# Optimization experiments

Measured on AMD Instinct MI355X. Metric: run time of the kernel, lower is better.

The kernel has to match this reference:

```python
import jax, jax.numpy as jnp
import numpy as np

B, S, D, H, L, F = 1, 2048, 768, 12, 2, 3072
DH = D // H          # 64
W = 256              # one-sided sliding window (attention_window=512 total)
NC = S // W          # number of query chunks
VOCAB = 50265


def _ln(x, s, b, eps=1e-5):
    m = x.mean(-1, keepdims=True)
    v = ((x - m) ** 2).mean(-1, keepdims=True)
    return (x - m) / jnp.sqrt(v + eps) * s + b


def setup_inputs() -> dict:
    key = jax.random.key(0)
    ks = jax.random.split(key, 16)
    p = lambda k, sh: jax.random.normal(k, sh, jnp.float32) * 0.02
    return {
        "input_ids": jax.random.randint(ks[0], (B, S), 0, VOCAB),
        "attention_mask": jnp.ones((B, S), jnp.int32),
        "word_emb": p(ks[1], (VOCAB, D)),
        "pos_emb": p(ks[2], (S + 2, D)),          # roberta-style pos ids start at 2
        "type_emb": p(ks[3], (1, D)),
        "emb_ln_s": jnp.ones((D,), jnp.float32),
        "emb_ln_b": jnp.zeros((D,), jnp.float32),
        "Wqkv": p(ks[4], (L, 3, D, D)),
        "bqkv": jnp.zeros((L, 3, D), jnp.float32),
        "Wo": p(ks[5], (L, D, D)),
        "bo": jnp.zeros((L, D), jnp.float32),
        "ln1_s": jnp.ones((L, D), jnp.float32),
        "ln1_b": jnp.zeros((L, D), jnp.float32),
        "W1": p(ks[6], (L, D, F)),
        "b1": jnp.zeros((L, F), jnp.float32),
        "W2": p(ks[7], (L, F, D)),
        "b2": jnp.zeros((L, D), jnp.float32),
        "ln2_s": jnp.ones((L, D), jnp.float32),
        "ln2_b": jnp.zeros((L, D), jnp.float32),
        "pool_W": p(ks[8], (D, D)),
        "pool_b": jnp.zeros((D,), jnp.float32),
    }


def reference(input_ids, attention_mask, word_emb, pos_emb, type_emb,
              emb_ln_s, emb_ln_b, Wqkv, bqkv, Wo, bo, ln1_s, ln1_b,
              W1, b1, W2, b2, ln2_s, ln2_b, pool_W, pool_b):
    # ---- embeddings (roberta/longformer style) ----
    pos_ids = jnp.cumsum(attention_mask, axis=1) * attention_mask + 1  # padding_idx=1
    x = word_emb[input_ids] + pos_emb[pos_ids] + type_emb[0]
    x = _ln(x, emb_ln_s, emb_ln_b)

    # ---- banded-attention index/mask precompute (int constants) ----
    idx = jnp.arange(NC)[:, None] * W + jnp.arange(3 * W)[None, :]      # [NC, 3W] into padded seq
    rel = (jnp.arange(3 * W)[None, :] - W) - jnp.arange(W)[:, None]     # key_pos - query_pos
    band = (rel >= -W) & (rel <= W)                                      # [W, 3W]
    kmask = jnp.pad(attention_mask, ((0, 0), (W, W)))[:, idx].astype(bool)  # [B, NC, 3W]
    valid = band[None, None] & kmask[:, :, None, :]                      # [B, NC, W, 3W]

    inv_sqrt_dh = 1.0 / np.sqrt(DH)
    for l in range(L):
        qkv = jnp.einsum('bsd,tde->tbse', x, Wqkv[l]) + bqkv[l][:, None, None, :]
        q, k, v = [t.reshape(B, S, H, DH).transpose(0, 2, 1, 3) for t in qkv]  # [B,H,S,DH]
        qc = q.reshape(B, H, NC, W, DH)
        kp = jnp.pad(k, ((0, 0), (0, 0), (W, W), (0, 0)))
        vp = jnp.pad(v, ((0, 0), (0, 0), (W, W), (0, 0)))
        kc = kp[:, :, idx]                                               # [B,H,NC,3W,DH]
        vc = vp[:, :, idx]
        scores = jnp.einsum('bhcqd,bhckd->bhcqk', qc, kc) * inv_sqrt_dh  # [B,H,NC,W,3W]
        scores = jnp.where(valid[:, None], scores, -1e9)
        attn = jax.nn.softmax(scores, axis=-1)
        ctx = jnp.einsum('bhcqk,bhckd->bhcqd', attn, vc)
        ctx = ctx.reshape(B, H, S, DH).transpose(0, 2, 1, 3).reshape(B, S, D)
        x = _ln(x + ctx @ Wo[l] + bo[l], ln1_s[l], ln1_b[l])
        h = jax.nn.gelu(x @ W1[l] + b1[l], approximate=False)
        x = _ln(x + h @ W2[l] + b2[l], ln2_s[l], ln2_b[l])

    pooled = jnp.tanh(x[:, 0] @ pool_W + pool_b)
    return x, pooled
```

## Files before the change

### kernel.cpp

```cpp
#include <hip/hip_runtime.h>
#include <hip/hip_bf16.h>
#include <math.h>
#include <stddef.h>
#include <stdint.h>

typedef __hip_bfloat16 bf16;
typedef short bf16x8 __attribute__((ext_vector_type(8)));
typedef float f32x4 __attribute__((ext_vector_type(4)));

#define CS 2048
#define CD 768
#define CH 12
#define CDH 64
#define CF 3072
#define CW 256
#define CL 2
#define QKVN 2304
#define SDC ((size_t)CS * CD)

__device__ __forceinline__ void gload_lds16(const bf16* g, bf16* l) {
  __builtin_amdgcn_global_load_lds(
      (const __attribute__((address_space(1))) void*)g,
      (__attribute__((address_space(3))) void*)l, 16, 0, 0);
}

__device__ __forceinline__ unsigned short f2bu(float v) {
  bf16 b = __float2bfloat16(v);
  return *(unsigned short*)&b;
}

__device__ __forceinline__ float block_reduce_sum(float v, float* buf) {
  #pragma unroll
  for (int off = 32; off > 0; off >>= 1) v += __shfl_down(v, off, 64);
  int wid = threadIdx.x >> 6;
  __syncthreads();
  if ((threadIdx.x & 63) == 0) buf[wid] = v;
  __syncthreads();
  if (threadIdx.x == 0) buf[0] = buf[0] + buf[1] + buf[2] + buf[3];
  __syncthreads();
  return buf[0];
}

__global__ __launch_bounds__(256) void transpose_all(
    const float* __restrict__ Wqkv, const float* __restrict__ Wo,
    const float* __restrict__ W1, const float* __restrict__ W2,
    bf16* __restrict__ WqkvT, bf16* __restrict__ WoT,
    bf16* __restrict__ W1T, bf16* __restrict__ W2T) {
  __shared__ float tile[32][33];
  int b = blockIdx.x;
  const float* src; bf16* dst; int K, N, t;
  if (b < 3456) {
    int mat = b / 576; t = b % 576; K = 768; N = 768;
    src = Wqkv + (size_t)mat * 768 * 768; dst = WqkvT + (size_t)mat * 768 * 768;
  } else if (b < 4608) {
    b -= 3456; int mat = b / 576; t = b % 576; K = 768; N = 768;
    src = Wo + (size_t)mat * 768 * 768; dst = WoT + (size_t)mat * 768 * 768;
  } else if (b < 9216) {
    b -= 4608; int mat = b / 2304; t = b % 2304; K = 768; N = 3072;
    src = W1 + (size_t)mat * 768 * 3072; dst = W1T + (size_t)mat * 768 * 3072;
  } else {
    b -= 9216; int mat = b / 2304; t = b % 2304; K = 3072; N = 768;
    src = W2 + (size_t)mat * 3072 * 768; dst = W2T + (size_t)mat * 3072 * 768;
  }
  int nt = N / 32;
  int bn = (t % nt) * 32, bk = (t / nt) * 32;
  int tx = threadIdx.x & 31, ty = (threadIdx.x >> 5) & 7;
  #pragma unroll
  for (int i = 0; i < 32; i += 8)
    tile[ty + i][tx] = src[(size_t)(bk + ty + i) * N + bn + tx];
  __syncthreads();
  #pragma unroll
  for (int i = 0; i < 32; i += 8)
    dst[(size_t)(bn + ty + i) * K + bk + tx] = __float2bfloat16(tile[tx][ty + i]);
}

__global__ __launch_bounds__(256) void embed_ln_kernel(
    const int* __restrict__ ids, const int* __restrict__ mask,
    const float* __restrict__ wemb, const float* __restrict__ pemb,
    const float* __restrict__ temb, const float* __restrict__ gs,
    const float* __restrict__ gb, float* __restrict__ x, bf16* __restrict__ xb) {
  __shared__ float red[4];
  int srow = blockIdx.x;
  float ps = 0.f;
  for (int i = threadIdx.x; i <= srow; i += 256) ps += (float)mask[i];
  float tot = block_reduce_sum(ps, red);
  long long pid = (long long)((int)(tot + 0.5f) * mask[srow] + 1);
  long long id = ids[srow];
  float v[3];
  #pragma unroll
  for (int i = 0; i < 3; ++i) {
    int d = threadIdx.x + i * 256;
    v[i] = wemb[id * CD + d] + pemb[pid * CD + d] + temb[d];
  }
  float sum = v[0] + v[1] + v[2];
  sum = block_reduce_sum(sum, red);
  float mean = sum * (1.0f / CD);
  float sq = 0.f;
  #pragma unroll
  for (int i = 0; i < 3; ++i) { float c = v[i] - mean; sq += c * c; }
  sq = block_reduce_sum(sq, red);
  float rstd = rsqrtf(sq * (1.0f / CD) + 1e-5f);
  #pragma unroll
  for (int i = 0; i < 3; ++i) {
    int d = threadIdx.x + i * 256;
    float o = (v[i] - mean) * rstd * gs[d] + gb[d];
    x[(size_t)srow * CD + d] = o;
    xb[(size_t)srow * CD + d] = __float2bfloat16(o);
  }
}

template<int GELU, int OUTBF16, int SPLITS, int VTFUSE>
__global__ __launch_bounds__(256) void gemm_mfma(
    const bf16* __restrict__ A, const bf16* __restrict__ Bt,
    const float* __restrict__ bias, void* __restrict__ Cout,
    bf16* __restrict__ vTout, int M, int N, int Ktot) {
  __shared__ __align__(16) bf16 As[128 * 64];
  __shared__ __align__(16) bf16 Bs[128 * 64];
  const int tid = threadIdx.x;
  const int wave = tid >> 6, lane = tid & 63;
  const int m0 = blockIdx.y * 128, n0 = blockIdx.x * 128;
  const int wm = (wave & 1) * 64, wn = (wave >> 1) * 64;
  const int quad = lane >> 4, rsel = lane & 15;
  const int rx = rsel & 7;
  const int r_in = lane >> 3;
  const int chunk = lane & 7;
  const int gchunk = chunk ^ r_in;
  const int Klen = Ktot / SPLITS;
  const int koff = (SPLITS > 1) ? blockIdx.z * Klen : 0;

  f32x4 acc[4][4] = {};

  for (int k0 = 0; k0 < Klen; k0 += 64) {
    #pragma unroll
    for (int i = 0; i < 8; ++i) {
      int op = wave * 8 + i;
      if (op < 16) {
        int row = op * 8 + r_in;
        gload_lds16(A + (size_t)(m0 + row) * Ktot + koff + k0 + gchunk * 8, &As[op * 512]);
      } else {
        int row = (op - 16) * 8 + r_in;
        gload_lds16(Bt + (size_t)(n0 + row) * Ktot + koff + k0 + gchunk * 8, &Bs[(op - 16) * 512]);
      }
    }
    __syncthreads();
    #pragma unroll
    for (int kh = 0; kh < 2; ++kh) {
      bf16x8 af[4], bfr[4];
      int cq = ((kh << 2) | quad);
      #pragma unroll
      for (int i = 0; i < 4; ++i)
        af[i] = *(const bf16x8*)&As[(wm + i * 16 + rsel) * 64 + (cq ^ rx) * 8];
      #pragma unroll
      for (int j = 0; j < 4; ++j)
        bfr[j] = *(const bf16x8*)&Bs[(wn + j * 16 + rsel) * 64 + (cq ^ rx) * 8];
      #pragma unroll
      for (int i = 0; i < 4; ++i)
        #pragma unroll
        for (int j = 0; j < 4; ++j)
          acc[i][j] = __builtin_amdgcn_mfma_f32_16x16x32_bf16(af[i], bfr[j], acc[i][j], 0, 0, 0);
    }
    __syncthreads();
  }
  #pragma unroll
  for (int j = 0; j < 4; ++j) {
    int col = n0 + wn + j * 16 + rsel;
    float bv = (SPLITS == 1 || blockIdx.z == 0) ? bias[col] : 0.f;
    if (VTFUSE && col >= 1536) {
      #pragma unroll
      for (int i = 0; i < 4; ++i) {
        int rowb = m0 + wm + i * 16 + quad * 4;
        ushort4 pk;
        pk.x = f2bu(acc[i][j][0] + bv);
        pk.y = f2bu(acc[i][j][1] + bv);
        pk.z = f2bu(acc[i][j][2] + bv);
        pk.w = f2bu(acc[i][j][3] + bv);
        *(ushort4*)&vTout[(size_t)(col - 1536) * CS + rowb] = pk;
      }
    } else {
      #pragma unroll
      for (int i = 0; i < 4; ++i) {
        #pragma unroll
        for (int r = 0; r < 4; ++r) {
          int rowm = m0 + wm + i * 16 + quad * 4 + r;
          float v = acc[i][j][r] + bv;
          if (GELU) v = 0.5f * v * (1.0f + erff(v * 0.70710678118654752f));
          if (SPLITS > 1)
            ((bf16*)Cout)[(size_t)blockIdx.z * M * N + (size_t)rowm * N + col] = __float2bfloat16(v);
          else if (OUTBF16)
            ((bf16*)Cout)[(size_t)rowm * N + col] = __float2bfloat16(v);
          else
            ((float*)Cout)[(size_t)rowm * N + col] = v;
        }
      }
    }
  }
}

__global__ __launch_bounds__(512) void attn_mfma(
    const bf16* __restrict__ qkv, const bf16* __restrict__ vT,
    const int* __restrict__ mask, bf16* __restrict__ ctx) {
  __shared__ bf16 Ps[8][16][72];
  __shared__ float Obuf[4][16][64];
  __shared__ float Mbuf[4][16];
  __shared__ float Lbuf[4][16];
  const int h = blockIdx.y;
  const int q0 = blockIdx.x * 64;
  const int tid = threadIdx.x;
  const int wv = tid >> 6, lane = tid & 63;
  const int qg = wv & 3, half = wv >> 2;
  const int quad = lane >> 4, rsel = lane & 15;
  const int qw = q0 + qg * 16;

  const bf16* qp = &qkv[(size_t)(qw + rsel) * QKVN + h * CDH + quad * 8];
  bf16x8 qf0 = *(const bf16x8*)qp;
  bf16x8 qf1 = *(const bf16x8*)(qp + 32);

  float mi[4], li[4];
  f32x4 o[4] = {};
  #pragma unroll
  for (int r = 0; r < 4; ++r) { mi[r] = -1e30f; li[r] = 0.f; }

  const int kt0 = half ? 5 : 0, kt1 = half ? 9 : 5;
  #pragma unroll 1
  for (int kt = kt0; kt < kt1; ++kt) {
    int kbase = qw - CW + kt * 64;
    if (kbase + 63 < 0 || kbase >= CS) continue;

    f32x4 sc[4];
    #pragma unroll
    for (int nt = 0; nt < 4; ++nt) {
      int pp = kbase + nt * 16 + rsel;
      int ppc = min(max(pp, 0), CS - 1);
      const bf16* kp = &qkv[(size_t)ppc * QKVN + 768 + h * CDH + quad * 8];
      bf16x8 kf0 = *(const bf16x8*)kp;
      bf16x8 kf1 = *(const bf16x8*)(kp + 32);
      f32x4 z = {};
      z = __builtin_amdgcn_mfma_f32_16x16x32_bf16(qf0, kf0, z, 0, 0, 0);
      z = __builtin_amdgcn_mfma_f32_16x16x32_bf16(qf1, kf1, z, 0, 0, 0);
      sc[nt] = z;
    }
    float mx[4] = {-1e30f, -1e30f, -1e30f, -1e30f};
    #pragma unroll
    for (int nt = 0; nt < 4; ++nt) {
      int pp = kbase + nt * 16 + rsel;
      int ppc = min(max(pp, 0), CS - 1);
      bool kvld = (pp >= 0) && (pp < CS) && (mask[ppc] != 0);
      #pragma unroll
      for (int r = 0; r < 4; ++r) {
        int qr = qw + quad * 4 + r;
        float s = sc[nt][r] * 0.125f;
        bool band = (pp >= qr - CW) && (pp <= qr + CW);
        s = (kvld && band) ? s : -1e9f;
        sc[nt][r] = s;
        mx[r] = fmaxf(mx[r], s);
      }
    }
    #pragma unroll
    for (int r = 0; r < 4; ++r) {
      #pragma unroll
      for (int off = 1; off < 16; off <<= 1)
        mx[r] = fmaxf(mx[r], __shfl_xor(mx[r], off, 64));
    }
    float al[4], rs[4] = {};
    #pragma unroll
    for (int r = 0; r < 4; ++r) {
      float mn = fmaxf(mi[r], mx[r]);
      al[r] = __expf(mi[r] - mn);
      mi[r] = mn;
    }
    #pragma unroll
    for (int nt = 0; nt < 4; ++nt)
      #pragma unroll
      for (int r = 0; r < 4; ++r) {
        float p = __expf(sc[nt][r] - mi[r]);
        sc[nt][r] = p;
        rs[r] += p;
      }
    #pragma unroll
    for (int r = 0; r < 4; ++r) {
      #pragma unroll
      for (int off = 1; off < 16; off <<= 1)
        rs[r] += __shfl_xor(rs[r], off, 64);
      li[r] = li[r] * al[r] + rs[r];
    }
    #pragma unroll
    for (int d = 0; d < 4; ++d)
      #pragma unroll
      for (int r = 0; r < 4; ++r) o[d][r] *= al[r];
    #pragma unroll
    for (int nt = 0; nt < 4; ++nt)
      #pragma unroll
      for (int r = 0; r < 4; ++r)
        Ps[wv][quad * 4 + r][nt * 16 + rsel] = __float2bfloat16(sc[nt][r]);
    __asm__ volatile("s_waitcnt lgkmcnt(0)" ::: "memory");
    bf16x8 pf0 = *(const bf16x8*)&Ps[wv][rsel][quad * 8];
    bf16x8 pf1 = *(const bf16x8*)&Ps[wv][rsel][32 + quad * 8];
    int kc0 = min(max(kbase + quad * 8, 0), CS - 8);
    int kc1 = min(max(kbase + 32 + quad * 8, 0), CS - 8);
    #pragma unroll
    for (int d = 0; d < 4; ++d) {
      const bf16* vrow = &vT[(size_t)(h * CDH + d * 16 + rsel) * CS];
      bf16x8 vf0 = *(const bf16x8*)(vrow + kc0);
      bf16x8 vf1 = *(const bf16x8*)(vrow + kc1);
      o[d] = __builtin_amdgcn_mfma_f32_16x16x32_bf16(pf0, vf0, o[d], 0, 0, 0);
      o[d] = __builtin_amdgcn_mfma_f32_16x16x32_bf16(pf1, vf1, o[d], 0, 0, 0);
    }
  }

  if (half == 1) {
    #pragma unroll
    for (int d = 0; d < 4; ++d)
      #pragma unroll
      for (int r = 0; r < 4; ++r)
        Obuf[qg][quad * 4 + r][d * 16 + rsel] = o[d][r];
    if (rsel == 0) {
      #pragma unroll
      for (int r = 0; r < 4; ++r) {
        Mbuf[qg][quad * 4 + r] = mi[r];
        Lbuf[qg][quad * 4 + r] = li[r];
      }
    }
  }
  __syncthreads();
  if (half == 0) {
    #pragma unroll
    for (int r = 0; r < 4; ++r) {
      int row = quad * 4 + r;
      float m1 = Mbuf[qg][row], l1 = Lbuf[qg][row];
      float mn = fmaxf(mi[r], m1);
      float a0 = __expf(mi[r] - mn);
      float a1 = __expf(m1 - mn);
      float inv = 1.0f / (li[r] * a0 + l1 * a1);
      #pragma unroll
      for (int d = 0; d < 4; ++d) {
        float val = (o[d][r] * a0 + Obuf[qg][row][d * 16 + rsel] * a1) * inv;
        ctx[(size_t)(qw + row) * CD + h * CDH + d * 16 + rsel] = __float2bfloat16(val);
      }
    }
  }
}

template<int P>
__global__ __launch_bounds__(256) void add_ln_kernel(
    const bf16* __restrict__ g, const float* __restrict__ xin,
    float* __restrict__ xout, bf16* __restrict__ xb,
    const float* __restrict__ gs, const float* __restrict__ gb) {
  __shared__ float red[4];
  int srow = blockIdx.x;
  float v[3];
  #pragma unroll
  for (int i = 0; i < 3; ++i) {
    int d = threadIdx.x + i * 256;
    size_t idx = (size_t)srow * CD + d;
    float a = xin[idx];
    #pragma unroll
    for (int p = 0; p < P; ++p) a += __bfloat162float(g[p * SDC + idx]);
    v[i] = a;
  }
  float sum = v[0] + v[1] + v[2];
  sum = block_reduce_sum(sum, red);
  float mean = sum * (1.0f / CD);
  float sq = 0.f;
  #pragma unroll
  for (int i = 0; i < 3; ++i) { float c = v[i] - mean; sq += c * c; }
  sq = block_reduce_sum(sq, red);
  float rstd = rsqrtf(sq * (1.0f / CD) + 1e-5f);
  #pragma unroll
  for (int i = 0; i < 3; ++i) {
    int d = threadIdx.x + i * 256;
    float o = (v[i] - mean) * rstd * gs[d] + gb[d];
    xout[(size_t)srow * CD + d] = o;
    xb[(size_t)srow * CD + d] = __float2bfloat16(o);
  }
}

__global__ __launch_bounds__(256) void pool_kernel(
    const float* __restrict__ x, const float* __restrict__ Wp,
    const float* __restrict__ bp, float* __restrict__ out) {
  __shared__ float xs[CD];
  __shared__ float red[4][64];
  int t = threadIdx.x;
  for (int i = t; i < CD; i += 256) xs[i] = x[i];
  __syncthreads();
  int n = blockIdx.x * 64 + (t & 63);
  int kp = t >> 6;
  float acc = 0.f;
  #pragma unroll 4
  for (int kk = kp * 192; kk < kp * 192 + 192; ++kk)
    acc = fmaf(xs[kk], Wp[(size_t)kk * CD + n], acc);
  red[kp][t & 63] = acc;
  __syncthreads();
  if (t < 64) {
    int nn = blockIdx.x * 64 + t;
    out[nn] = tanhf(red[0][t] + red[1][t] + red[2][t] + red[3][t] + bp[nn]);
  }
}

extern "C" void kernel_launch(void* const* d_in, const int* in_sizes, int n_in,
                              void* d_out, int out_size, void* d_ws, size_t ws_size,
                              hipStream_t stream) {
  const int*   ids   = (const int*)d_in[0];
  const int*   mask  = (const int*)d_in[1];
  const float* wemb  = (const float*)d_in[2];
  const float* pemb  = (const float*)d_in[3];
  const float* temb  = (const float*)d_in[4];
  const float* elns  = (const float*)d_in[5];
  const float* elnb  = (const float*)d_in[6];
  const float* Wqkv  = (const float*)d_in[7];
  const float* bqkv  = (const float*)d_in[8];
  const float* Wo    = (const float*)d_in[9];
  const float* bo    = (const float*)d_in[10];
  const float* ln1s  = (const float*)d_in[11];
  const float* ln1b  = (const float*)d_in[12];
  const float* W1    = (const float*)d_in[13];
  const float* b1    = (const float*)d_in[14];
  const float* W2    = (const float*)d_in[15];
  const float* b2    = (const float*)d_in[16];
  const float* ln2s  = (const float*)d_in[17];
  const float* ln2b  = (const float*)d_in[18];
  const float* poolW = (const float*)d_in[19];
  const float* poolb = (const float*)d_in[20];

  const size_t SD = SDC;
  const size_t SF = (size_t)CS * CF;

  char* w = (char*)d_ws;
  float* x    = (float*)w; w += SD * 4;
  bf16*  xb   = (bf16*)w;  w += SD * 2;
  bf16*  qkv  = (bf16*)w;  w += (size_t)CS * QKVN * 2;
  bf16*  vT   = (bf16*)w;  w += SD * 2;
  bf16*  ctxb = (bf16*)w;  w += SD * 2;
  bf16*  t1b  = (bf16*)w;  w += SF * 2;
  bf16*  t2   = (bf16*)w;  w += SD * 2 * 4;
  bf16* WqkvT = (bf16*)w;  w += (size_t)CL * QKVN * CD * 2;
  bf16* WoT   = (bf16*)w;  w += (size_t)CL * CD * CD * 2;
  bf16* W1T   = (bf16*)w;  w += (size_t)CL * CF * CD * 2;
  bf16* W2T   = (bf16*)w;  w += (size_t)CL * CD * CF * 2;

  transpose_all<<<13824, 256, 0, stream>>>(Wqkv, Wo, W1, W2, WqkvT, WoT, W1T, W2T);
  embed_ln_kernel<<<CS, 256, 0, stream>>>(ids, mask, wemb, pemb, temb, elns, elnb, x, xb);

  for (int l = 0; l < CL; ++l) {
    gemm_mfma<0,1,1,1><<<dim3(QKVN/128, CS/128), 256, 0, stream>>>(
        xb, WqkvT + (size_t)l * QKVN * CD, bqkv + (size_t)l * 3 * CD, qkv, vT, CS, QKVN, CD);
    attn_mfma<<<dim3(CS/64, CH), 512, 0, stream>>>(qkv, vT, mask, ctxb);
    gemm_mfma<0,0,2,0><<<dim3(CD/128, CS/128, 2), 256, 0, stream>>>(
        ctxb, WoT + (size_t)l * CD * CD, bo + (size_t)l * CD, t2, nullptr, CS, CD, CD);
    add_ln_kernel<2><<<CS, 256, 0, stream>>>(t2, x, x, xb,
        ln1s + (size_t)l * CD, ln1b + (size_t)l * CD);
    gemm_mfma<1,1,1,0><<<dim3(CF/128, CS/128), 256, 0, stream>>>(
        xb, W1T + (size_t)l * CF * CD, b1 + (size_t)l * CF, t1b, nullptr, CS, CF, CD);
    gemm_mfma<0,0,4,0><<<dim3(CD/128, CS/128, 4), 256, 0, stream>>>(
        t1b, W2T + (size_t)l * CD * CF, b2 + (size_t)l * CD, t2, nullptr, CS, CD, CF);
    float* lastx = (l == CL - 1) ? (float*)d_out : x;
    add_ln_kernel<4><<<CS, 256, 0, stream>>>(t2, x, lastx, xb,
        ln2s + (size_t)l * CD, ln2b + (size_t)l * CD);
  }

  pool_kernel<<<12, 256, 0, stream>>>((float*)d_out, poolW, poolb, (float*)d_out + SD);
}
```

Baseline: 557.7 us.

## Merge prep kernels, stage GEMM and attention epilogues through LDS, vectorise LayerNorm

Merges the weight transpose and the embedding LayerNorm into a single prep launch. GEMM epilogues now go through an LDS tile so each row is written with 16-byte stores, and the MFMA operands are swapped so each lane holds four consecutive columns. The attention context output is staged in LDS the same way, and s_setprio is placed around the MFMAs. The LayerNorm kernels move to 192 threads with float4 loads and stores and one fewer barrier in the reduction. Together these aim to cut uncoalesced scalar global writes and launch overhead, at the cost of extra LDS traffic and barriers in the epilogues.

```diff
diff --git a/kernel.cpp b/kernel.cpp
--- a/kernel.cpp
+++ b/kernel.cpp
@@ -17,6 +17,7 @@
 #define CL 2
 #define QKVN 2304
 #define SDC ((size_t)CS * CD)
+#define EPS_LD 136
 
 __device__ __forceinline__ void gload_lds16(const bf16* g, bf16* l) {
   __builtin_amdgcn_global_load_lds(
@@ -28,94 +29,109 @@
   bf16 b = __float2bfloat16(v);
   return *(unsigned short*)&b;
 }
-
+__device__ __forceinline__ float bu2f(unsigned short u) {
+  bf16 b = *(bf16*)&u;
+  return __bfloat162float(b);
+}
+
+template<int NW>
 __device__ __forceinline__ float block_reduce_sum(float v, float* buf) {
   #pragma unroll
   for (int off = 32; off > 0; off >>= 1) v += __shfl_down(v, off, 64);
-  int wid = threadIdx.x >> 6;
   __syncthreads();
-  if ((threadIdx.x & 63) == 0) buf[wid] = v;
+  if ((threadIdx.x & 63) == 0) buf[threadIdx.x >> 6] = v;
   __syncthreads();
-  if (threadIdx.x == 0) buf[0] = buf[0] + buf[1] + buf[2] + buf[3];
-  __syncthreads();
-  return buf[0];
-}
-
-__global__ __launch_bounds__(256) void transpose_all(
+  float s = buf[0];
+  #pragma unroll
+  for (int w = 1; w < NW; ++w) s += buf[w];
+  return s;
+}
+
+__global__ __launch_bounds__(256) void prep_kernel(
     const float* __restrict__ Wqkv, const float* __restrict__ Wo,
     const float* __restrict__ W1, const float* __restrict__ W2,
     bf16* __restrict__ WqkvT, bf16* __restrict__ WoT,
-    bf16* __restrict__ W1T, bf16* __restrict__ W2T) {
-  __shared__ float tile[32][33];
-  int b = blockIdx.x;
-  const float* src; bf16* dst; int K, N, t;
-  if (b < 3456) {
-    int mat = b / 576; t = b % 576; K = 768; N = 768;
-    src = Wqkv + (size_t)mat * 768 * 768; dst = WqkvT + (size_t)mat * 768 * 768;
-  } else if (b < 4608) {
-    b -= 3456; int mat = b / 576; t = b % 576; K = 768; N = 768;
-    src = Wo + (size_t)mat * 768 * 768; dst = WoT + (size_t)mat * 768 * 768;
-  } else if (b < 9216) {
-    b -= 4608; int mat = b / 2304; t = b % 2304; K = 768; N = 3072;
-    src = W1 + (size_t)mat * 768 * 3072; dst = W1T + (size_t)mat * 768 * 3072;
-  } else {
-    b -= 9216; int mat = b / 2304; t = b % 2304; K = 3072; N = 768;
-    src = W2 + (size_t)mat * 3072 * 768; dst = W2T + (size_t)mat * 3072 * 768;
-  }
-  int nt = N / 32;
-  int bn = (t % nt) * 32, bk = (t / nt) * 32;
-  int tx = threadIdx.x & 31, ty = (threadIdx.x >> 5) & 7;
-  #pragma unroll
-  for (int i = 0; i < 32; i += 8)
-    tile[ty + i][tx] = src[(size_t)(bk + ty + i) * N + bn + tx];
-  __syncthreads();
-  #pragma unroll
-  for (int i = 0; i < 32; i += 8)
-    dst[(size_t)(bn + ty + i) * K + bk + tx] = __float2bfloat16(tile[tx][ty + i]);
-}
-
-__global__ __launch_bounds__(256) void embed_ln_kernel(
+    bf16* __restrict__ W1T, bf16* __restrict__ W2T,
     const int* __restrict__ ids, const int* __restrict__ mask,
     const float* __restrict__ wemb, const float* __restrict__ pemb,
     const float* __restrict__ temb, const float* __restrict__ gs,
     const float* __restrict__ gb, float* __restrict__ x, bf16* __restrict__ xb) {
+  __shared__ float tile[32][33];
   __shared__ float red[4];
-  int srow = blockIdx.x;
-  float ps = 0.f;
-  for (int i = threadIdx.x; i <= srow; i += 256) ps += (float)mask[i];
-  float tot = block_reduce_sum(ps, red);
-  long long pid = (long long)((int)(tot + 0.5f) * mask[srow] + 1);
-  long long id = ids[srow];
-  float v[3];
-  #pragma unroll
-  for (int i = 0; i < 3; ++i) {
-    int d = threadIdx.x + i * 256;
-    v[i] = wemb[id * CD + d] + pemb[pid * CD + d] + temb[d];
-  }
-  float sum = v[0] + v[1] + v[2];
-  sum = block_reduce_sum(sum, red);
-  float mean = sum * (1.0f / CD);
-  float sq = 0.f;
-  #pragma unroll
-  for (int i = 0; i < 3; ++i) { float c = v[i] - mean; sq += c * c; }
-  sq = block_reduce_sum(sq, red);
-  float rstd = rsqrtf(sq * (1.0f / CD) + 1e-5f);
-  #pragma unroll
-  for (int i = 0; i < 3; ++i) {
-    int d = threadIdx.x + i * 256;
-    float o = (v[i] - mean) * rstd * gs[d] + gb[d];
-    x[(size_t)srow * CD + d] = o;
-    xb[(size_t)srow * CD + d] = __float2bfloat16(o);
-  }
-}
-
-template<int GELU, int OUTBF16, int SPLITS, int VTFUSE>
-__global__ __launch_bounds__(256) void gemm_mfma(
+  int b = blockIdx.x;
+  if (b < 13824) {
+    const float* src; bf16* dst; int K, N, t;
+    if (b < 3456) {
+      int mat = b / 576; t = b % 576; K = 768; N = 768;
+      src = Wqkv + (size_t)mat * 768 * 768; dst = WqkvT + (size_t)mat * 768 * 768;
+    } else if (b < 4608) {
+      b -= 3456; int mat = b / 576; t = b % 576; K = 768; N = 768;
+      src = Wo + (size_t)mat * 768 * 768; dst = WoT + (size_t)mat * 768 * 768;
+    } else if (b < 9216) {
+      b -= 4608; int mat = b / 2304; t = b % 2304; K = 768; N = 3072;
+      src = W1 + (size_t)mat * 768 * 3072; dst = W1T + (size_t)mat * 768 * 3072;
+    } else {
+      b -= 9216; int mat = b / 2304; t = b % 2304; K = 3072; N = 768;
+      src = W2 + (size_t)mat * 3072 * 768; dst = W2T + (size_t)mat * 3072 * 768;
+    }
+    int nt = N / 32;
+    int bn = (t % nt) * 32, bk = (t / nt) * 32;
+    int tx = threadIdx.x & 31, ty = (threadIdx.x >> 5) & 7;
+    #pragma unroll
+    for (int i = 0; i < 32; i += 8)
+      tile[ty + i][tx] = src[(size_t)(bk + ty + i) * N + bn + tx];
+    __syncthreads();
+    #pragma unroll
+    for (int i = 0; i < 32; i += 8)
+      dst[(size_t)(bn + ty + i) * K + bk + tx] = __float2bfloat16(tile[tx][ty + i]);
+  } else {
+    int srow = b - 13824;
+    int t = threadIdx.x;
+    float ps = 0.f;
+    for (int i = t; i <= srow; i += 256) ps += (float)mask[i];
+    float tot = block_reduce_sum<4>(ps, red);
+    long long pid = (long long)((int)(tot + 0.5f) * mask[srow] + 1);
+    long long id = ids[srow];
+    float4 v = {0.f, 0.f, 0.f, 0.f};
+    if (t < 192) {
+      int d = t * 4;
+      float4 a = *(const float4*)&wemb[id * CD + d];
+      float4 p = *(const float4*)&pemb[pid * CD + d];
+      float4 tm = *(const float4*)&temb[d];
+      v.x = a.x + p.x + tm.x; v.y = a.y + p.y + tm.y;
+      v.z = a.z + p.z + tm.z; v.w = a.w + p.w + tm.w;
+    }
+    float sum = block_reduce_sum<4>(v.x + v.y + v.z + v.w, red);
+    float mean = sum * (1.0f / CD);
+    float cx = v.x - mean, cy = v.y - mean, cz = v.z - mean, cw = v.w - mean;
+    float sqv = (t < 192) ? (cx * cx + cy * cy + cz * cz + cw * cw) : 0.f;
+    float sq = block_reduce_sum<4>(sqv, red);
+    float rstd = rsqrtf(sq * (1.0f / CD) + 1e-5f);
+    if (t < 192) {
+      int d = t * 4;
+      float4 g4 = *(const float4*)&gs[d];
+      float4 b4 = *(const float4*)&gb[d];
+      float4 o;
+      o.x = cx * rstd * g4.x + b4.x;
+      o.y = cy * rstd * g4.y + b4.y;
+      o.z = cz * rstd * g4.z + b4.z;
+      o.w = cw * rstd * g4.w + b4.w;
+      *(float4*)&x[(size_t)srow * CD + d] = o;
+      ushort4 pk;
+      pk.x = f2bu(o.x); pk.y = f2bu(o.y); pk.z = f2bu(o.z); pk.w = f2bu(o.w);
+      *(ushort4*)&xb[(size_t)srow * CD + d] = pk;
+    }
+  }
+}
+
+template<int GELU, int SPLITS, int TRANS>
+__device__ __forceinline__ void gemm_body(
     const bf16* __restrict__ A, const bf16* __restrict__ Bt,
-    const float* __restrict__ bias, void* __restrict__ Cout,
-    bf16* __restrict__ vTout, int M, int N, int Ktot) {
-  __shared__ __align__(16) bf16 As[128 * 64];
-  __shared__ __align__(16) bf16 Bs[128 * 64];
+    const float* __restrict__ bias, bf16* __restrict__ Cout,
+    bf16* __restrict__ vTout, int M, int N, int Ktot, char* smem) {
+  bf16* As = (bf16*)smem;
+  bf16* Bs = (bf16*)(smem + 128 * 64 * 2);
+  bf16* eps = (bf16*)smem;
   const int tid = threadIdx.x;
   const int wave = tid >> 6, lane = tid & 63;
   const int m0 = blockIdx.y * 128, n0 = blockIdx.x * 128;
@@ -156,50 +172,89 @@
       #pragma unroll
       for (int i = 0; i < 4; ++i)
         #pragma unroll
-        for (int j = 0; j < 4; ++j)
-          acc[i][j] = __builtin_amdgcn_mfma_f32_16x16x32_bf16(af[i], bfr[j], acc[i][j], 0, 0, 0);
+        for (int j = 0; j < 4; ++j) {
+          if (TRANS)
+            acc[i][j] = __builtin_amdgcn_mfma_f32_16x16x32_bf16(af[i], bfr[j], acc[i][j], 0, 0, 0);
+          else
+            acc[i][j] = __builtin_amdgcn_mfma_f32_16x16x32_bf16(bfr[j], af[i], acc[i][j], 0, 0, 0);
+        }
     }
     __syncthreads();
   }
-  #pragma unroll
-  for (int j = 0; j < 4; ++j) {
-    int col = n0 + wn + j * 16 + rsel;
-    float bv = (SPLITS == 1 || blockIdx.z == 0) ? bias[col] : 0.f;
-    if (VTFUSE && col >= 1536) {
+
+  if (!TRANS) {
+    #pragma unroll
+    for (int j = 0; j < 4; ++j) {
+      int cb = wn + j * 16 + quad * 4;
+      float4 bv = {0.f, 0.f, 0.f, 0.f};
+      if (SPLITS == 1 || blockIdx.z == 0) bv = *(const float4*)&bias[n0 + cb];
       #pragma unroll
       for (int i = 0; i < 4; ++i) {
-        int rowb = m0 + wm + i * 16 + quad * 4;
+        float v0 = acc[i][j][0] + bv.x;
+        float v1 = acc[i][j][1] + bv.y;
+        float v2 = acc[i][j][2] + bv.z;
+        float v3 = acc[i][j][3] + bv.w;
+        if (GELU) {
+          v0 = 0.5f * v0 * (1.0f + erff(v0 * 0.70710678118654752f));
+          v1 = 0.5f * v1 * (1.0f + erff(v1 * 0.70710678118654752f));
+          v2 = 0.5f * v2 * (1.0f + erff(v2 * 0.70710678118654752f));
+          v3 = 0.5f * v3 * (1.0f + erff(v3 * 0.70710678118654752f));
+        }
+        ushort4 pk;
+        pk.x = f2bu(v0); pk.y = f2bu(v1); pk.z = f2bu(v2); pk.w = f2bu(v3);
+        *(ushort4*)&eps[(wm + i * 16 + rsel) * EPS_LD + cb] = pk;
+      }
+    }
+    __syncthreads();
+    const size_t zb = (SPLITS > 1) ? (size_t)blockIdx.z * M * N : 0;
+    #pragma unroll
+    for (int it = 0; it < 8; ++it) {
+      int row = it * 16 + (tid >> 4);
+      int c = tid & 15;
+      bf16x8 v = *(const bf16x8*)&eps[row * EPS_LD + c * 8];
+      *(bf16x8*)&Cout[zb + (size_t)(m0 + row) * N + n0 + c * 8] = v;
+    }
+  } else {
+    #pragma unroll
+    for (int j = 0; j < 4; ++j) {
+      float bv = bias[n0 + wn + j * 16 + rsel];
+      #pragma unroll
+      for (int i = 0; i < 4; ++i) {
         ushort4 pk;
         pk.x = f2bu(acc[i][j][0] + bv);
         pk.y = f2bu(acc[i][j][1] + bv);
         pk.z = f2bu(acc[i][j][2] + bv);
         pk.w = f2bu(acc[i][j][3] + bv);
-        *(ushort4*)&vTout[(size_t)(col - 1536) * CS + rowb] = pk;
-      }
-    } else {
-      #pragma unroll
-      for (int i = 0; i < 4; ++i) {
-        #pragma unroll
-        for (int r = 0; r < 4; ++r) {
-          int rowm = m0 + wm + i * 16 + quad * 4 + r;
-          float v = acc[i][j][r] + bv;
-          if (GELU) v = 0.5f * v * (1.0f + erff(v * 0.70710678118654752f));
-          if (SPLITS > 1)
-            ((bf16*)Cout)[(size_t)blockIdx.z * M * N + (size_t)rowm * N + col] = __float2bfloat16(v);
-          else if (OUTBF16)
-            ((bf16*)Cout)[(size_t)rowm * N + col] = __float2bfloat16(v);
-          else
-            ((float*)Cout)[(size_t)rowm * N + col] = v;
-        }
-      }
-    }
-  }
+        *(ushort4*)&eps[(wn + j * 16 + rsel) * EPS_LD + wm + i * 16 + quad * 4] = pk;
+      }
+    }
+    __syncthreads();
+    #pragma unroll
+    for (int it = 0; it < 8; ++it) {
+      int row = it * 16 + (tid >> 4);
+      int c = tid & 15;
+      bf16x8 v = *(const bf16x8*)&eps[row * EPS_LD + c * 8];
+      *(bf16x8*)&vTout[(size_t)(n0 - 1536 + row) * CS + m0 + c * 8] = v;
+    }
+  }
+}
+
+template<int GELU, int SPLITS, int VTFUSE>
+__global__ __launch_bounds__(256) void gemm_mfma(
+    const bf16* __restrict__ A, const bf16* __restrict__ Bt,
+    const float* __restrict__ bias, bf16* __restrict__ Cout,
+    bf16* __restrict__ vTout, int M, int N, int Ktot) {
+  __shared__ __align__(16) char smem[128 * EPS_LD * 2];
+  if (VTFUSE && blockIdx.x * 128 >= 1536)
+    gemm_body<0, 1, 1>(A, Bt, bias, Cout, vTout, M, N, Ktot, smem);
+  else
+    gemm_body<GELU, SPLITS, 0>(A, Bt, bias, Cout, vTout, M, N, Ktot, smem);
 }
 
 __global__ __launch_bounds__(512) void attn_mfma(
     const bf16* __restrict__ qkv, const bf16* __restrict__ vT,
     const int* __restrict__ mask, bf16* __restrict__ ctx) {
-  __shared__ bf16 Ps[8][16][72];
+  __shared__ __align__(16) bf16 Ps[8][16][72];
   __shared__ float Obuf[4][16][64];
   __shared__ float Mbuf[4][16];
   __shared__ float Lbuf[4][16];
@@ -235,8 +290,10 @@
       bf16x8 kf0 = *(const bf16x8*)kp;
       bf16x8 kf1 = *(const bf16x8*)(kp + 32);
       f32x4 z = {};
+      __builtin_amdgcn_s_setprio(1);
       z = __builtin_amdgcn_mfma_f32_16x16x32_bf16(qf0, kf0, z, 0, 0, 0);
       z = __builtin_amdgcn_mfma_f32_16x16x32_bf16(qf1, kf1, z, 0, 0, 0);
+      __builtin_amdgcn_s_setprio(0);
       sc[nt] = z;
     }
     float mx[4] = {-1e30f, -1e30f, -1e30f, -1e30f};
@@ -302,8 +359,10 @@
       const bf16* vrow = &vT[(size_t)(h * CDH + d * 16 + rsel) * CS];
       bf16x8 vf0 = *(const bf16x8*)(vrow + kc0);
       bf16x8 vf1 = *(const bf16x8*)(vrow + kc1);
+      __builtin_amdgcn_s_setprio(1);
       o[d] = __builtin_amdgcn_mfma_f32_16x16x32_bf16(pf0, vf0, o[d], 0, 0, 0);
       o[d] = __builtin_amdgcn_mfma_f32_16x16x32_bf16(pf1, vf1, o[d], 0, 0, 0);
+      __builtin_amdgcn_s_setprio(0);
     }
   }
 
@@ -323,6 +382,7 @@
   }
   __syncthreads();
   if (half == 0) {
+    bf16* Cs = &Ps[qg][0][0];
     #pragma unroll
     for (int r = 0; r < 4; ++r) {
       int row = quad * 4 + r;
@@ -334,44 +394,49 @@
       #pragma unroll
       for (int d = 0; d < 4; ++d) {
         float val = (o[d][r] * a0 + Obuf[qg][row][d * 16 + rsel] * a1) * inv;
-        ctx[(size_t)(qw + row) * CD + h * CDH + d * 16 + rsel] = __float2bfloat16(val);
-      }
-    }
+        Cs[row * 72 + d * 16 + rsel] = __float2bfloat16(val);
+      }
+    }
+  }
+  __syncthreads();
+  {
+    int qg2 = tid >> 7, rr = (tid >> 3) & 15, cc = tid & 7;
+    bf16x8 vv = *(const bf16x8*)&Ps[qg2][rr][cc * 8];
+    *(bf16x8*)&ctx[(size_t)(q0 + qg2 * 16 + rr) * CD + h * CDH + cc * 8] = vv;
   }
 }
 
 template<int P>
-__global__ __launch_bounds__(256) void add_ln_kernel(
+__global__ __launch_bounds__(192) void add_ln_kernel(
     const bf16* __restrict__ g, const float* __restrict__ xin,
     float* __restrict__ xout, bf16* __restrict__ xb,
     const float* __restrict__ gs, const float* __restrict__ gb) {
-  __shared__ float red[4];
+  __shared__ float red[3];
   int srow = blockIdx.x;
-  float v[3];
+  int d = threadIdx.x * 4;
+  size_t base = (size_t)srow * CD + d;
+  float4 a = *(const float4*)&xin[base];
   #pragma unroll
-  for (int i = 0; i < 3; ++i) {
-    int d = threadIdx.x + i * 256;
-    size_t idx = (size_t)srow * CD + d;
-    float a = xin[idx];
-    #pragma unroll
-    for (int p = 0; p < P; ++p) a += __bfloat162float(g[p * SDC + idx]);
-    v[i] = a;
-  }
-  float sum = v[0] + v[1] + v[2];
-  sum = block_reduce_sum(sum, red);
+  for (int p = 0; p < P; ++p) {
+    ushort4 gg = *(const ushort4*)&g[p * SDC + base];
+    a.x += bu2f(gg.x); a.y += bu2f(gg.y); a.z += bu2f(gg.z); a.w += bu2f(gg.w);
+  }
+  float sum = block_reduce_sum<3>(a.x + a.y + a.z + a.w, red);
   float mean = sum * (1.0f / CD);
-  float sq = 0.f;
-  #pragma unroll
-  for (int i = 0; i < 3; ++i) { float c = v[i] - mean; sq += c * c; }
-  sq = block_reduce_sum(sq, red);
+  float cx = a.x - mean, cy = a.y - mean, cz = a.z - mean, cw = a.w - mean;
+  float sq = block_reduce_sum<3>(cx * cx + cy * cy + cz * cz + cw * cw, red);
   float rstd = rsqrtf(sq * (1.0f / CD) + 1e-5f);
-  #pragma unroll
-  for (int i = 0; i < 3; ++i) {
-    int d = threadIdx.x + i * 256;
-    float o = (v[i] - mean) * rstd * gs[d] + gb[d];
-    xout[(size_t)srow * CD + d] = o;
-    xb[(size_t)srow * CD + d] = __float2bfloat16(o);
-  }
+  float4 g4 = *(const float4*)&gs[d];
+  float4 b4 = *(const float4*)&gb[d];
+  float4 o;
+  o.x = cx * rstd * g4.x + b4.x;
+  o.y = cy * rstd * g4.y + b4.y;
+  o.z = cz * rstd * g4.z + b4.z;
+  o.w = cw * rstd * g4.w + b4.w;
+  *(float4*)&xout[base] = o;
+  ushort4 pk;
+  pk.x = f2bu(o.x); pk.y = f2bu(o.y); pk.z = f2bu(o.z); pk.w = f2bu(o.w);
+  *(ushort4*)&xb[base] = pk;
 }
 
 __global__ __launch_bounds__(256) void pool_kernel(
@@ -437,23 +502,24 @@
   bf16* W1T   = (bf16*)w;  w += (size_t)CL * CF * CD * 2;
   bf16* W2T   = (bf16*)w;  w += (size_t)CL * CD * CF * 2;
 
-  transpose_all<<<13824, 256, 0, stream>>>(Wqkv, Wo, W1, W2, WqkvT, WoT, W1T, W2T);
-  embed_ln_kernel<<<CS, 256, 0, stream>>>(ids, mask, wemb, pemb, temb, elns, elnb, x, xb);
+  prep_kernel<<<13824 + CS, 256, 0, stream>>>(
+      Wqkv, Wo, W1, W2, WqkvT, WoT, W1T, W2T,
+      ids, mask, wemb, pemb, temb, elns, elnb, x, xb);
 
   for (int l = 0; l < CL; ++l) {
-    gemm_mfma<0,1,1,1><<<dim3(QKVN/128, CS/128), 256, 0, stream>>>(
+    gemm_mfma<0,1,1><<<dim3(QKVN/128, CS/128), 256, 0, stream>>>(
         xb, WqkvT + (size_t)l * QKVN * CD, bqkv + (size_t)l * 3 * CD, qkv, vT, CS, QKVN, CD);
     attn_mfma<<<dim3(CS/64, CH), 512, 0, stream>>>(qkv, vT, mask, ctxb);
-    gemm_mfma<0,0,2,0><<<dim3(CD/128, CS/128, 2), 256, 0, stream>>>(
+    gemm_mfma<0,2,0><<<dim3(CD/128, CS/128, 2), 256, 0, stream>>>(
         ctxb, WoT + (size_t)l * CD * CD, bo + (size_t)l * CD, t2, nullptr, CS, CD, CD);
-    add_ln_kernel<2><<<CS, 256, 0, stream>>>(t2, x, x, xb,
+    add_ln_kernel<2><<<CS, 192, 0, stream>>>(t2, x, x, xb,
         ln1s + (size_t)l * CD, ln1b + (size_t)l * CD);
-    gemm_mfma<1,1,1,0><<<dim3(CF/128, CS/128), 256, 0, stream>>>(
+    gemm_mfma<1,1,0><<<dim3(CF/128, CS/128), 256, 0, stream>>>(
         xb, W1T + (size_t)l * CF * CD, b1 + (size_t)l * CF, t1b, nullptr, CS, CF, CD);
-    gemm_mfma<0,0,4,0><<<dim3(CD/128, CS/128, 4), 256, 0, stream>>>(
+    gemm_mfma<0,4,0><<<dim3(CD/128, CS/128, 4), 256, 0, stream>>>(
         t1b, W2T + (size_t)l * CD * CF, b2 + (size_t)l * CD, t2, nullptr, CS, CD, CF);
     float* lastx = (l == CL - 1) ? (float*)d_out : x;
-    add_ln_kernel<4><<<CS, 256, 0, stream>>>(t2, x, lastx, xb,
+    add_ln_kernel<4><<<CS, 192, 0, stream>>>(t2, x, lastx, xb,
         ln2s + (size_t)l * CD, ln2b + (size_t)l * CD);
   }
 
```

New measurement: 553.1 us. Within noise of the previous version (-0.8%).
